# Kernel tuning notes

Hardware: AMD Instinct MI355X
Metric: run time of the kernel (lower is better)

## Reference

```python
import jax, jax.numpy as jnp
import numpy as np
from jax import lax

B, N, F, HID = 32, 1000, 16, 64
HIST, FC = 24, 24
DEG = 16
E = B * N * DEG  # 512000 edges in block-diagonal batched graph
GC_IN = F + 2          # conv input: xn(1) + y(1) + X(F)
GRU_IN_ENC = GC_IN + HID


def setup_inputs() -> dict:
    key = jax.random.key(0)
    ks = jax.random.split(key, 24)
    X = jax.random.normal(ks[0], (B, HIST + FC, N, F), jnp.float32)
    y = jax.random.normal(ks[1], (B, HIST + FC, N, 1), jnp.float32)
    # edges stay within each batch's graph (dense_to_sparse of batch-repeated adj)
    src_local = jax.random.randint(ks[2], (B, N * DEG), 0, N)
    dst_local = jnp.tile(jnp.repeat(jnp.arange(N), DEG)[None, :], (B, 1))
    offs = (jnp.arange(B) * N)[:, None]
    edge_index = jnp.stack([(src_local + offs).reshape(-1),
                            (dst_local + offs).reshape(-1)], 0).astype(jnp.int32)
    edge_weight = jax.random.uniform(ks[3], (E,), jnp.float32)
    s = 0.1
    p = {
        'W_rel': s * jax.random.normal(ks[4], (GC_IN, HID), jnp.float32),
        'b_rel': jnp.zeros((HID,), jnp.float32),
        'W_root': s * jax.random.normal(ks[5], (GC_IN, HID), jnp.float32),
        'enc_Wih': s * jax.random.normal(ks[6], (3 * HID, GRU_IN_ENC), jnp.float32),
        'enc_Whh': s * jax.random.normal(ks[7], (3 * HID, HID), jnp.float32),
        'enc_bih': jnp.zeros((3 * HID,), jnp.float32),
        'enc_bhh': jnp.zeros((3 * HID,), jnp.float32),
        'enc_Wout': s * jax.random.normal(ks[8], (HID, 1), jnp.float32),
        'enc_bout': jnp.zeros((1,), jnp.float32),
        'dec_Win': s * jax.random.normal(ks[9], (4, HID), jnp.float32),
        'dec_bin': jnp.zeros((HID,), jnp.float32),
        'dec_Wih': s * jax.random.normal(ks[10], (3 * HID, HID), jnp.float32),
        'dec_Whh': s * jax.random.normal(ks[11], (3 * HID, HID), jnp.float32),
        'dec_bih': jnp.zeros((3 * HID,), jnp.float32),
        'dec_bhh': jnp.zeros((3 * HID,), jnp.float32),
        'dec_Wout': s * jax.random.normal(ks[12], (HID, 1), jnp.float32),
        'dec_bout': jnp.zeros((1,), jnp.float32),
    }
    return dict(X=X, y=y, edge_index=edge_index, edge_weight=edge_weight, **p)


def _gru_cell(x, h, Wih, Whh, bih, bhh):
    gi = x @ Wih.T + bih
    gh = h @ Whh.T + bhh
    ir, iz, inn = jnp.split(gi, 3, axis=-1)
    hr, hz, hnn = jnp.split(gh, 3, axis=-1)
    r = jax.nn.sigmoid(ir + hr)
    z = jax.nn.sigmoid(iz + hz)
    n = jnp.tanh(inn + r * hnn)
    return (1.0 - z) * n + z * h


def reference(X, y, edge_index, edge_weight,
              W_rel, b_rel, W_root,
              enc_Wih, enc_Whh, enc_bih, enc_bhh, enc_Wout, enc_bout,
              dec_Win, dec_bin, dec_Wih, dec_Whh, dec_bih, dec_bhh, dec_Wout, dec_bout):
    src, dst = edge_index[0], edge_index[1]

    def enc_step(carry, inp):
        hn, xn = carry          # hn: [B*N, HID], xn: [B, N, 1]
        X_t, y_t = inp          # [B,N,F], [B,N,1]
        x = jnp.concatenate([xn, y_t, X_t], axis=-1)   # [B,N,F+2]
        xg = x.reshape(B * N, GC_IN)
        msg = edge_weight[:, None] * xg[src]           # gather
        agg = jax.ops.segment_sum(msg, dst, num_segments=B * N)  # scatter-add
        conv = jax.nn.sigmoid(agg @ W_rel + b_rel + xg @ W_root)  # GraphConv
        xfull = jnp.concatenate([xg, conv], axis=-1)   # [B*N, F+2+HID]
        hn = _gru_cell(xfull, hn, enc_Wih, enc_Whh, enc_bih, enc_bhh)
        xn = hn.reshape(B, N, HID) @ enc_Wout + enc_bout
        return (hn, xn), None

    h0 = jnp.zeros((B * N, HID), X.dtype)
    xn0 = jnp.zeros((B, N, 1), X.dtype)
    X_enc = jnp.moveaxis(X[:, :HIST], 1, 0)   # [HIST,B,N,F]
    y_enc = jnp.moveaxis(y[:, :HIST], 1, 0)
    (hn, xn), _ = lax.scan(enc_step, (h0, xn0), (X_enc, y_enc))

    def dec_step(carry, X_t):
        hn, xn = carry
        x = jnp.concatenate([xn, X_t], axis=-1).reshape(B * N, 4)
        x = x @ dec_Win + dec_bin
        hn = _gru_cell(x, hn, dec_Wih, dec_Whh, dec_bih, dec_bhh)
        xn = hn.reshape(B, N, HID) @ dec_Wout + dec_bout
        return (hn, xn), xn

    X_dec = jnp.moveaxis(X[:, HIST:, :, -3:], 1, 0)  # [FC,B,N,3]
    _, preds = lax.scan(dec_step, (hn, xn), X_dec)
    return jnp.moveaxis(preds, 0, 1)                 # [B, FC, N, 1]
```

## Files before the change

kernel.cpp:

```cpp
#include <hip/hip_runtime.h>
#include <cstdint>

#define BX   32
#define NN   1000
#define FF   16
#define TT   48
#define HIST 24
#define FC   24
#define HID  64
#define DEG  16
#define BN   (BX*NN)
#define IMGP 40

typedef __attribute__((ext_vector_type(8)))  short s8v;
typedef __attribute__((ext_vector_type(16))) float f16v;

__device__ __forceinline__ float sigf(float x)  { return 1.0f/(1.0f+__expf(-x)); }
__device__ __forceinline__ float tanhf_(float x){ return 2.0f/(1.0f+__expf(-2.0f*x)) - 1.0f; }
__device__ __forceinline__ unsigned short f2bf(float x){
    unsigned int u = __float_as_uint(x);
    return (unsigned short)((u + 0x7FFFu + ((u>>16)&1u)) >> 16);
}
__device__ __forceinline__ float bf2f(unsigned short b){
    return __uint_as_float(((unsigned int)b)<<16);
}
__device__ __forceinline__ unsigned int cvtpk(float a, float b){
    unsigned int r;
    asm("v_cvt_pk_bf16_f32 %0, %1, %2" : "=v"(r) : "v"(a), "v"(b));
    return r;
}

__device__ __forceinline__ void  xn_st(float* p, float v){
    __hip_atomic_store(p, v, __ATOMIC_RELAXED, __HIP_MEMORY_SCOPE_AGENT);
}
__device__ __forceinline__ float xn_ld(const float* p){
    return __hip_atomic_load(p, __ATOMIC_RELAXED, __HIP_MEMORY_SCOPE_AGENT);
}

__device__ __forceinline__ void batch_barrier(unsigned int* bar, unsigned int target){
    __syncthreads();
    if (threadIdx.x == 0){
        asm volatile("s_waitcnt vmcnt(0)" ::: "memory");
        __hip_atomic_fetch_add(bar, 1u, __ATOMIC_RELAXED, __HIP_MEMORY_SCOPE_AGENT);
        while (__hip_atomic_load(bar, __ATOMIC_RELAXED, __HIP_MEMORY_SCOPE_AGENT) < target)
            __builtin_amdgcn_s_sleep(1);
    }
    __syncthreads();
}

__global__ void prep_weights(
    const float* __restrict__ W_rel, const float* __restrict__ W_root,
    const float* __restrict__ eWih, const float* __restrict__ eWhh,
    const float* __restrict__ dWih, const float* __restrict__ dWhh,
    unsigned short* __restrict__ encB, unsigned short* __restrict__ decB)
{
    const int i = blockIdx.x*256 + threadIdx.x;
    if (i < 64*56){
        int n = i/56, k = i%56;
        float v = 0.f;
        if (k < 17)                 v = W_rel[(k+1)*64 + n];
        else if (k == 17)           v = W_root[64 + n];
        else if (k >= 18 && k < 34) v = W_root[(k-16)*64 + n];
        else if (k == 34)           v = W_rel[n];
        else if (k == 35)           v = W_root[n];
        encB[i] = f2bf(v);
    }
    if (i < 192*96){
        int n = i/96, c = i%96;
        float v = 0.f;
        if (c >= 1 && c <= 17)       v = eWih[n*82 + c];
        else if (c == 19)            v = eWih[n*82 + 0];
        else if (c >= 32 && c < 96)  v = eWih[n*82 + 18 + (c-32)];
        encB[3584 + i] = f2bf(v);
    }
    if (i < 192*72){
        int n = i/72, k = i%72;
        encB[22016 + i] = f2bf((k < 64) ? eWhh[n*64 + k] : 0.f);
        decB[i]         = f2bf((k < 64) ? dWih[n*64 + k] : 0.f);
        decB[13824 + i] = f2bf((k < 64) ? dWhh[n*64 + k] : 0.f);
    }
}

__global__ __launch_bounds__(1024, 4) void agg_pre(
    const float* __restrict__ X, const float* __restrict__ y,
    const int*   __restrict__ esrc, const float* __restrict__ ew,
    unsigned short* __restrict__ img)
{
    extern __shared__ float sm[];
    float* Xs = sm;
    float* ys = sm + NN*FF;

    const int b = blockIdx.x;
    const int t = blockIdx.y;
    const float* Xt = X + (size_t)(b*TT + t)*NN*FF;
    const float* yt = y + (size_t)(b*TT + t)*NN;

    for (int i = threadIdx.x; i < NN*FF/4; i += 1024)
        ((float4*)Xs)[i] = ((const float4*)Xt)[i];
    for (int i = threadIdx.x; i < NN; i += 1024)
        ys[i] = yt[i];
    __syncthreads();

    const int nl = threadIdx.x;
    const int nc = (nl < NN) ? nl : NN-1;
    const int node = b*NN + nc;
    float a[18];
    #pragma unroll
    for (int i=0;i<17;i++) a[i]=0.f;
    const int4*   sv = (const int4*)  (esrc + node*DEG);
    const float4* wv = (const float4*)(ew   + node*DEG);
    #pragma unroll
    for (int q=0;q<4;q++){
        int4 s4 = sv[q]; float4 w4 = wv[q];
        const int   ss[4] = {s4.x, s4.y, s4.z, s4.w};
        const float ww[4] = {w4.x, w4.y, w4.z, w4.w};
        #pragma unroll
        for (int i=0;i<4;i++){
            const int sl = ss[i] - b*NN;
            const float wgt = ww[i];
            a[0] += wgt * ys[sl];
            const float4* sr = (const float4*)&Xs[sl*FF];
            #pragma unroll
            for (int q2=0;q2<4;q2++){
                float4 v = sr[q2];
                a[1+4*q2] += wgt*v.x; a[2+4*q2] += wgt*v.y;
                a[3+4*q2] += wgt*v.z; a[4+4*q2] += wgt*v.w;
            }
        }
    }
    a[17] = ys[nc];
    const int gblk = b*8 + (nl >> 7);
    unsigned int* w32 = (unsigned int*)(img +
        (((size_t)t*256 + gblk)*128 + (nl & 127))*IMGP);
    #pragma unroll
    for (int p=0;p<9;p++)  w32[p]   = cvtpk(a[2*p], a[2*p+1]);
    #pragma unroll
    for (int p=0;p<8;p++)  w32[9+p] = cvtpk(Xs[nc*FF+2*p], Xs[nc*FF+2*p+1]);
}

#define OFFB1   0
#define OFFBIH  3584
#define OFFBHH  22016
#define DOFFBIH 0
#define DOFFBHH 13824
#define OFFAS   35840
#define OFFAHB  53248
#define OFFHF   124928
#define FU_SMEM 159744
#define PAS  136
#define PB1  56
#define PBIH 96
#define PB72 72
#define PHF  68

__global__ __launch_bounds__(512, 1) void fused_steps(
    const float* __restrict__ X,
    const int* __restrict__ esrc, const float* __restrict__ ew,
    const unsigned short* __restrict__ img,
    const unsigned short* __restrict__ encB, const unsigned short* __restrict__ decB,
    const float* __restrict__ b_rel,
    const float* __restrict__ ebih, const float* __restrict__ ebhh,
    const float* __restrict__ eWout, const float* __restrict__ ebout,
    const float* __restrict__ dbih, const float* __restrict__ dbhh,
    const float* __restrict__ dWin, const float* __restrict__ dbin,
    const float* __restrict__ dWout, const float* __restrict__ dbout,
    float* __restrict__ xnA, float* __restrict__ xnB,
    unsigned int* __restrict__ bar, float* __restrict__ out)
{
    extern __shared__ char smraw[];
    __shared__ float xnL[128];
    unsigned short* sm16 = (unsigned short*)smraw;
    float* hf = (float*)(smraw + OFFHF);

    const int tid  = threadIdx.x;
    const int lane = tid & 63;
    const int w    = __builtin_amdgcn_readfirstlane(tid >> 6);
    const int mt = w >> 1, jt = w & 1;
    const int batch = blockIdx.x >> 3;
    const int sub   = blockIdx.x & 7;
    unsigned int* mybar = bar + batch*32;

    {
        const uint4* src = (const uint4*)encB;
        uint4* dst = (uint4*)smraw;
        for (int i = tid; i < 4480; i += 512) dst[i] = src[i];
        unsigned int* z32 = (unsigned int*)(smraw + 71680);
        for (int i = tid; i < 22016; i += 512) z32[i] = 0u;
    }

    for (int t = 0; t < TT; ++t){
        const bool enc = (t < HIST);
        const float* xn_r = (t & 1) ? xnB : xnA;
        float*       xn_w = (t & 1) ? xnA : xnB;

        if (enc){
            {
                const unsigned short* imgrow = img +
                    (((size_t)t*256 + blockIdx.x)*128)*IMGP;
                for (int i = tid; i < 640; i += 512){
                    int node = i/5, part = i - node*5;
                    if (part < 4){
                        uint4 v = *(const uint4*)(imgrow + node*IMGP + part*8);
                        *(uint4*)(sm16 + OFFAS + node*PAS + part*8) = v;
                    } else {
                        unsigned int v = *(const unsigned int*)(imgrow + node*IMGP + 32);
                        *(unsigned int*)(sm16 + OFFAS + node*PAS + 32) = v;
                    }
                }
            }
            if (tid < 128){
                const int nl2 = sub*128 + tid;
                const int nc  = (nl2 < NN) ? nl2 : NN-1;
                const int node_g = batch*NN + nc;
                float a0 = 0.f, xnv = 0.f;
                if (t > 0){
                    const int4*   sv = (const int4*)  (esrc + node_g*DEG);
                    const float4* wv = (const float4*)(ew   + node_g*DEG);
                    #pragma unroll
                    for (int q=0;q<4;q++){
                        int4 s4 = sv[q]; float4 w4 = wv[q];
                        a0 += w4.x*xn_ld(xn_r + s4.x) + w4.y*xn_ld(xn_r + s4.y)
                            + w4.z*xn_ld(xn_r + s4.z) + w4.w*xn_ld(xn_r + s4.w);
                    }
                    xnv = xn_ld(xn_r + node_g);
                }
                *(unsigned int*)(sm16 + OFFAS + tid*PAS + 34) = cvtpk(a0, xnv);
            }
            __syncthreads();

            {
                f16v acc = {};
                const int rA = mt*32 + (lane & 31);
                const int rB = jt*32 + (lane & 31);
                const int ke = (lane >> 5)*8;
                #pragma unroll
                for (int ks=0; ks<3; ks++){
                    s8v a = *(const s8v*)(sm16 + OFFAS + rA*PAS + ks*16 + ke);
                    s8v b = *(const s8v*)(sm16 + OFFB1 + rB*PB1 + ks*16 + ke);
                    acc = __builtin_amdgcn_mfma_f32_32x32x16_bf16(a, b, acc, 0, 0, 0);
                }
                const int j = jt*32 + (lane & 31);
                const float brl = b_rel[j];
                #pragma unroll
                for (int p=0; p<8; p++){
                    float s0 = sigf(acc[2*p]   + brl);
                    float s1 = sigf(acc[2*p+1] + brl);
                    unsigned int pk = cvtpk(s0, s1);
                    int row = ((2*p)&3) + 8*(p>>1) + 4*(lane>>5);
                    sm16[OFFAS + (mt*32 + row  )*PAS + 64 + j] = (unsigned short)pk;
                    sm16[OFFAS + (mt*32 + row+1)*PAS + 64 + j] = (unsigned short)(pk>>16);
                }
            }
            __syncthreads();

            f16v accx[3] = {{},{},{}};
            f16v acch[3] = {{},{},{}};
            {
                const int rA = mt*32 + (lane & 31);
                const int ln = lane & 31;
                const int ke = (lane >> 5)*8;
                #pragma unroll
                for (int s=0; s<6; s++){
                    const int acol = (s < 2) ? (16 + 16*s) : (32 + 16*s);
                    s8v a = *(const s8v*)(sm16 + OFFAS + rA*PAS + acol + ke);
                    #pragma unroll
                    for (int nt=0; nt<3; nt++){
                        int NT = jt + nt*2;
                        s8v b = *(const s8v*)(sm16 + OFFBIH + (NT*32 + ln)*PBIH + s*16 + ke);
                        accx[nt] = __builtin_amdgcn_mfma_f32_32x32x16_bf16(a, b, accx[nt], 0,0,0);
                    }
                }
                #pragma unroll
                for (int ks=0; ks<4; ks++){
                    s8v ah = *(const s8v*)(sm16 + OFFAHB + rA*PB72 + ks*16 + ke);
                    #pragma unroll
                    for (int nt=0; nt<3; nt++){
                        int NT = jt + nt*2;
                        s8v b = *(const s8v*)(sm16 + OFFBHH + (NT*32 + ln)*PB72 + ks*16 + ke);
                        acch[nt] = __builtin_amdgcn_mfma_f32_32x32x16_bf16(ah, b, acch[nt], 0,0,0);
                    }
                }
            }
            __syncthreads();

            {
                const int j = jt*32 + (lane & 31);
                const float br  = ebih[j]     + ebhh[j];
                const float bz  = ebih[64+j]  + ebhh[64+j];
                const float bin_ = ebih[128+j];
                const float bhn  = ebhh[128+j];
                #pragma unroll
                for (int p=0; p<8; p++){
                    const int r0 = 2*p, r1 = 2*p+1;
                    int row = ((r0)&3) + 8*(p>>1) + 4*(lane>>5);
                    const int n0 = mt*32 + row, n1 = n0 + 1;
                    float hold0 = hf[n0*PHF + j];
                    float hold1 = hf[n1*PHF + j];
                    float rr0 = sigf(accx[0][r0] + acch[0][r0] + br);
                    float rr1 = sigf(accx[0][r1] + acch[0][r1] + br);
                    float zz0 = sigf(accx[1][r0] + acch[1][r0] + bz);
                    float zz1 = sigf(accx[1][r1] + acch[1][r1] + bz);
                    float nn0 = tanhf_(accx[2][r0] + bin_ + rr0*(acch[2][r0] + bhn));
                    float nn1 = tanhf_(accx[2][r1] + bin_ + rr1*(acch[2][r1] + bhn));
                    float hp0 = (1.f - zz0)*nn0 + zz0*hold0;
                    float hp1 = (1.f - zz1)*nn1 + zz1*hold1;
                    hf[n0*PHF + j] = hp0;
                    hf[n1*PHF + j] = hp1;
                    unsigned int nh = cvtpk(hp0, hp1);
                    sm16[OFFAHB + n0*PB72 + j] = (unsigned short)nh;
                    sm16[OFFAHB + n1*PB72 + j] = (unsigned short)(nh>>16);
                }
            }
            __syncthreads();

            if (tid < 128){
                const float4* hv = (const float4*)(hf + tid*PHF);
                float s = ebout[0];
                #pragma unroll
                for (int q=0; q<16; q++){
                    float4 v = hv[q];
                    s += v.x*eWout[4*q] + v.y*eWout[4*q+1]
                       + v.z*eWout[4*q+2] + v.w*eWout[4*q+3];
                }
                const int nl2 = sub*128 + tid;
                if (nl2 < NN) xn_st(xn_w + batch*NN + nl2, s);
            }
        } else {
            if (t == HIST){
                const uint4* src = (const uint4*)decB;
                uint4* dst = (uint4*)smraw;
                for (int i = tid; i < 3456; i += 512) dst[i] = src[i];
            }
            {
                const int node = tid >> 2, c0 = (tid & 3)*16;
                const int nl2 = sub*128 + node;
                const int nc  = (nl2 < NN) ? nl2 : NN-1;
                const float* Xt = X + (size_t)(batch*TT + t)*NN*FF;
                float x0 = (t == HIST) ? xn_ld(xn_r + batch*NN + nc) : xnL[node];
                float x1 = Xt[nc*FF + 13];
                float x2 = Xt[nc*FF + 14];
                float x3 = Xt[nc*FF + 15];
                unsigned int* ax32 = (unsigned int*)(sm16 + OFFAS);
                #pragma unroll
                for (int p=0; p<8; p++){
                    int c = c0 + 2*p;
                    float va = dbin[c]   + x0*dWin[c]     + x1*dWin[64+c]   + x2*dWin[128+c]   + x3*dWin[192+c];
                    float vb = dbin[c+1] + x0*dWin[c+1]   + x1*dWin[64+c+1] + x2*dWin[128+c+1] + x3*dWin[192+c+1];
                    ax32[(node*PB72 + c) >> 1] = cvtpk(va, vb);
                }
            }
            __syncthreads();

            f16v accx[3] = {{},{},{}};
            f16v acch[3] = {{},{},{}};
            {
                const int rA = mt*32 + (lane & 31);
                const int ln = lane & 31;
                const int ke = (lane >> 5)*8;
                #pragma unroll
                for (int ks=0; ks<4; ks++){
                    s8v a = *(const s8v*)(sm16 + OFFAS + rA*PB72 + ks*16 + ke);
                    #pragma unroll
                    for (int nt=0; nt<3; nt++){
                        int NT = jt + nt*2;
                        s8v b = *(const s8v*)(sm16 + DOFFBIH + (NT*32 + ln)*PB72 + ks*16 + ke);
                        accx[nt] = __builtin_amdgcn_mfma_f32_32x32x16_bf16(a, b, accx[nt], 0,0,0);
                    }
                }
                #pragma unroll
                for (int ks=0; ks<4; ks++){
                    s8v ah = *(const s8v*)(sm16 + OFFAHB + rA*PB72 + ks*16 + ke);
                    #pragma unroll
                    for (int nt=0; nt<3; nt++){
                        int NT = jt + nt*2;
                        s8v b = *(const s8v*)(sm16 + DOFFBHH + (NT*32 + ln)*PB72 + ks*16 + ke);
                        acch[nt] = __builtin_amdgcn_mfma_f32_32x32x16_bf16(ah, b, acch[nt], 0,0,0);
                    }
                }
            }
            __syncthreads();

            {
                const int j = jt*32 + (lane & 31);
                const float br  = dbih[j]     + dbhh[j];
                const float bz  = dbih[64+j]  + dbhh[64+j];
                const float bin_ = dbih[128+j];
                const float bhn  = dbhh[128+j];
                #pragma unroll
                for (int p=0; p<8; p++){
                    const int r0 = 2*p, r1 = 2*p+1;
                    int row = ((r0)&3) + 8*(p>>1) + 4*(lane>>5);
                    const int n0 = mt*32 + row, n1 = n0 + 1;
                    float hold0 = hf[n0*PHF + j];
                    float hold1 = hf[n1*PHF + j];
                    float rr0 = sigf(accx[0][r0] + acch[0][r0] + br);
                    float rr1 = sigf(accx[0][r1] + acch[0][r1] + br);
                    float zz0 = sigf(accx[1][r0] + acch[1][r0] + bz);
                    float zz1 = sigf(accx[1][r1] + acch[1][r1] + bz);
                    float nn0 = tanhf_(accx[2][r0] + bin_ + rr0*(acch[2][r0] + bhn));
                    float nn1 = tanhf_(accx[2][r1] + bin_ + rr1*(acch[2][r1] + bhn));
                    float hp0 = (1.f - zz0)*nn0 + zz0*hold0;
                    float hp1 = (1.f - zz1)*nn1 + zz1*hold1;
                    hf[n0*PHF + j] = hp0;
                    hf[n1*PHF + j] = hp1;
                    unsigned int nh = cvtpk(hp0, hp1);
                    sm16[OFFAHB + n0*PB72 + j] = (unsigned short)nh;
                    sm16[OFFAHB + n1*PB72 + j] = (unsigned short)(nh>>16);
                }
            }
            __syncthreads();

            if (tid < 128){
                const float4* hv = (const float4*)(hf + tid*PHF);
                float s = dbout[0];
                #pragma unroll
                for (int q=0; q<16; q++){
                    float4 v = hv[q];
                    s += v.x*dWout[4*q] + v.y*dWout[4*q+1]
                       + v.z*dWout[4*q+2] + v.w*dWout[4*q+3];
                }
                xnL[tid] = s;
                const int nl2 = sub*128 + tid;
                if (nl2 < NN)
                    out[(size_t)(batch*FC + (t - HIST))*NN + nl2] = s;
            }
        }
        if (t < HIST-1) batch_barrier(mybar, 8u*(unsigned)(t+1));
        else            __syncthreads();
    }
}

extern "C" void kernel_launch(void* const* d_in, const int* in_sizes, int n_in,
                              void* d_out, int out_size, void* d_ws, size_t ws_size,
                              hipStream_t stream)
{
    const float* X     = (const float*)d_in[0];
    const float* y     = (const float*)d_in[1];
    const int*   ei    = (const int*)  d_in[2];
    const float* ew    = (const float*)d_in[3];
    const float* W_rel = (const float*)d_in[4];
    const float* b_rel = (const float*)d_in[5];
    const float* W_root= (const float*)d_in[6];
    const float* eWih  = (const float*)d_in[7];
    const float* eWhh  = (const float*)d_in[8];
    const float* ebih  = (const float*)d_in[9];
    const float* ebhh  = (const float*)d_in[10];
    const float* eWout = (const float*)d_in[11];
    const float* ebout = (const float*)d_in[12];
    const float* dWin  = (const float*)d_in[13];
    const float* dbin  = (const float*)d_in[14];
    const float* dWih  = (const float*)d_in[15];
    const float* dWhh  = (const float*)d_in[16];
    const float* dbih  = (const float*)d_in[17];
    const float* dbhh  = (const float*)d_in[18];
    const float* dWout = (const float*)d_in[19];
    const float* dbout = (const float*)d_in[20];
    float* out = (float*)d_out;

    unsigned short* img = (unsigned short*)d_ws;
    float* x0 = (float*)(img + (size_t)24*256*128*IMGP);
    float* x1 = x0 + BN;
    unsigned short* encB = (unsigned short*)(x1 + BN);
    unsigned short* decB = encB + 35840;
    unsigned int* bar = (unsigned int*)(decB + 27648);

    const int* esrc = ei;

    const int smA = (NN*FF + NN)*sizeof(float);
    hipFuncSetAttribute((const void*)agg_pre,
                        hipFuncAttributeMaxDynamicSharedMemorySize, smA);
    hipFuncSetAttribute((const void*)fused_steps,
                        hipFuncAttributeMaxDynamicSharedMemorySize, FU_SMEM);

    hipMemsetAsync(bar, 0, 32*32*sizeof(unsigned int), stream);
    prep_weights<<<78, 256, 0, stream>>>(W_rel, W_root, eWih, eWhh, dWih, dWhh, encB, decB);
    agg_pre<<<dim3(BX,24), 1024, smA, stream>>>(X, y, esrc, ew, img);

    void* args[] = {
        (void*)&X, (void*)&esrc, (void*)&ew, (void*)&img,
        (void*)&encB, (void*)&decB,
        (void*)&b_rel, (void*)&ebih, (void*)&ebhh, (void*)&eWout, (void*)&ebout,
        (void*)&dbih, (void*)&dbhh, (void*)&dWin, (void*)&dbin, (void*)&dWout, (void*)&dbout,
        (void*)&x0, (void*)&x1, (void*)&bar, (void*)&out
    };
    hipLaunchCooperativeKernel((const void*)fused_steps, dim3(256), dim3(512),
                               args, FU_SMEM, stream);
}
```

Baseline: 504.9 us.

## Prefetch next-step image tile, keep hidden state and edge lists in registers

Moves the per-step load of the encoder input tile out of the critical path: the next step's tile is loaded right after the GRU update barrier, so it overlaps with the output projection and the cross-block barrier. Edge source indices and weights are loaded once into registers instead of every step. The previous hidden state used by the GRU blend is kept in an MFMA-layout register vector rather than re-read from shared memory. In exchange, register pressure rises, which may reduce occupancy or cause spills. The early tile write must also not overlap any shared-memory reads still in flight.

```diff
diff --git a/kernel.cpp b/kernel.cpp
--- a/kernel.cpp
+++ b/kernel.cpp
@@ -188,41 +188,52 @@
         for (int i = tid; i < 22016; i += 512) z32[i] = 0u;
     }
 
+    f16v hreg = {};
+    int4 esv0={0,0,0,0}, esv1={0,0,0,0}, esv2={0,0,0,0}, esv3={0,0,0,0};
+    float4 ewv0={}, ewv1={}, ewv2={}, ewv3={};
+    int g_node = 0;
+    if (tid < 128){
+        const int nl2 = sub*128 + tid;
+        const int nc  = (nl2 < NN) ? nl2 : NN-1;
+        g_node = batch*NN + nc;
+        const int4*   sv = (const int4*)  (esrc + g_node*DEG);
+        const float4* wv = (const float4*)(ew   + g_node*DEG);
+        esv0=sv[0]; esv1=sv[1]; esv2=sv[2]; esv3=sv[3];
+        ewv0=wv[0]; ewv1=wv[1]; ewv2=wv[2]; ewv3=wv[3];
+    }
+    __syncthreads();
+
+    {
+        const unsigned short* imgrow = img + (((size_t)0*256 + blockIdx.x)*128)*IMGP;
+        {
+            int node = tid >> 2, part = tid & 3;
+            uint4 v = *(const uint4*)(imgrow + node*IMGP + part*8);
+            *(uint4*)(sm16 + OFFAS + node*PAS + part*8) = v;
+        }
+        if (tid < 128){
+            unsigned int v = *(const unsigned int*)(imgrow + tid*IMGP + 32);
+            *(unsigned int*)(sm16 + OFFAS + tid*PAS + 32) = v;
+        }
+    }
+
     for (int t = 0; t < TT; ++t){
         const bool enc = (t < HIST);
         const float* xn_r = (t & 1) ? xnB : xnA;
         float*       xn_w = (t & 1) ? xnA : xnB;
 
         if (enc){
-            {
-                const unsigned short* imgrow = img +
-                    (((size_t)t*256 + blockIdx.x)*128)*IMGP;
-                for (int i = tid; i < 640; i += 512){
-                    int node = i/5, part = i - node*5;
-                    if (part < 4){
-                        uint4 v = *(const uint4*)(imgrow + node*IMGP + part*8);
-                        *(uint4*)(sm16 + OFFAS + node*PAS + part*8) = v;
-                    } else {
-                        unsigned int v = *(const unsigned int*)(imgrow + node*IMGP + 32);
-                        *(unsigned int*)(sm16 + OFFAS + node*PAS + 32) = v;
-                    }
-                }
-            }
             if (tid < 128){
-                const int nl2 = sub*128 + tid;
-                const int nc  = (nl2 < NN) ? nl2 : NN-1;
-                const int node_g = batch*NN + nc;
                 float a0 = 0.f, xnv = 0.f;
                 if (t > 0){
-                    const int4*   sv = (const int4*)  (esrc + node_g*DEG);
-                    const float4* wv = (const float4*)(ew   + node_g*DEG);
-                    #pragma unroll
-                    for (int q=0;q<4;q++){
-                        int4 s4 = sv[q]; float4 w4 = wv[q];
-                        a0 += w4.x*xn_ld(xn_r + s4.x) + w4.y*xn_ld(xn_r + s4.y)
-                            + w4.z*xn_ld(xn_r + s4.z) + w4.w*xn_ld(xn_r + s4.w);
-                    }
-                    xnv = xn_ld(xn_r + node_g);
+                    a0 += ewv0.x*xn_ld(xn_r + esv0.x) + ewv0.y*xn_ld(xn_r + esv0.y)
+                        + ewv0.z*xn_ld(xn_r + esv0.z) + ewv0.w*xn_ld(xn_r + esv0.w);
+                    a0 += ewv1.x*xn_ld(xn_r + esv1.x) + ewv1.y*xn_ld(xn_r + esv1.y)
+                        + ewv1.z*xn_ld(xn_r + esv1.z) + ewv1.w*xn_ld(xn_r + esv1.w);
+                    a0 += ewv2.x*xn_ld(xn_r + esv2.x) + ewv2.y*xn_ld(xn_r + esv2.y)
+                        + ewv2.z*xn_ld(xn_r + esv2.z) + ewv2.w*xn_ld(xn_r + esv2.w);
+                    a0 += ewv3.x*xn_ld(xn_r + esv3.x) + ewv3.y*xn_ld(xn_r + esv3.y)
+                        + ewv3.z*xn_ld(xn_r + esv3.z) + ewv3.w*xn_ld(xn_r + esv3.w);
+                    xnv = xn_ld(xn_r + g_node);
                 }
                 *(unsigned int*)(sm16 + OFFAS + tid*PAS + 34) = cvtpk(a0, xnv);
             }
@@ -294,8 +305,8 @@
                     const int r0 = 2*p, r1 = 2*p+1;
                     int row = ((r0)&3) + 8*(p>>1) + 4*(lane>>5);
                     const int n0 = mt*32 + row, n1 = n0 + 1;
-                    float hold0 = hf[n0*PHF + j];
-                    float hold1 = hf[n1*PHF + j];
+                    float hold0 = hreg[r0];
+                    float hold1 = hreg[r1];
                     float rr0 = sigf(accx[0][r0] + acch[0][r0] + br);
                     float rr1 = sigf(accx[0][r1] + acch[0][r1] + br);
                     float zz0 = sigf(accx[1][r0] + acch[1][r0] + bz);
@@ -304,6 +315,8 @@
                     float nn1 = tanhf_(accx[2][r1] + bin_ + rr1*(acch[2][r1] + bhn));
                     float hp0 = (1.f - zz0)*nn0 + zz0*hold0;
                     float hp1 = (1.f - zz1)*nn1 + zz1*hold1;
+                    hreg[r0] = hp0;
+                    hreg[r1] = hp1;
                     hf[n0*PHF + j] = hp0;
                     hf[n1*PHF + j] = hp1;
                     unsigned int nh = cvtpk(hp0, hp1);
@@ -312,6 +325,20 @@
                 }
             }
             __syncthreads();
+
+            if (t+1 < HIST){
+                const unsigned short* imgrow = img +
+                    (((size_t)(t+1)*256 + blockIdx.x)*128)*IMGP;
+                {
+                    int node = tid >> 2, part = tid & 3;
+                    uint4 v = *(const uint4*)(imgrow + node*IMGP + part*8);
+                    *(uint4*)(sm16 + OFFAS + node*PAS + part*8) = v;
+                }
+                if (tid < 128){
+                    unsigned int v = *(const unsigned int*)(imgrow + tid*IMGP + 32);
+                    *(unsigned int*)(sm16 + OFFAS + tid*PAS + 32) = v;
+                }
+            }
 
             if (tid < 128){
                 const float4* hv = (const float4*)(hf + tid*PHF);
@@ -391,8 +418,8 @@
                     const int r0 = 2*p, r1 = 2*p+1;
                     int row = ((r0)&3) + 8*(p>>1) + 4*(lane>>5);
                     const int n0 = mt*32 + row, n1 = n0 + 1;
-                    float hold0 = hf[n0*PHF + j];
-                    float hold1 = hf[n1*PHF + j];
+                    float hold0 = hreg[r0];
+                    float hold1 = hreg[r1];
                     float rr0 = sigf(accx[0][r0] + acch[0][r0] + br);
                     float rr1 = sigf(accx[0][r1] + acch[0][r1] + br);
                     float zz0 = sigf(accx[1][r0] + acch[1][r0] + bz);
@@ -401,6 +428,8 @@
                     float nn1 = tanhf_(accx[2][r1] + bin_ + rr1*(acch[2][r1] + bhn));
                     float hp0 = (1.f - zz0)*nn0 + zz0*hold0;
                     float hp1 = (1.f - zz1)*nn1 + zz1*hold1;
+                    hreg[r0] = hp0;
+                    hreg[r1] = hp1;
                     hf[n0*PHF + j] = hp0;
                     hf[n1*PHF + j] = hp1;
                     unsigned int nh = cvtpk(hp0, hp1);
```

Measured after the change: 487.4 us. 1.04x faster.
